# Performance work log

Hardware: AMD Instinct MI355X
Metric: run time of the kernel (lower is better)

## Reference

```python
import jax, jax.numpy as jnp
import numpy as np

C, K, D = 256, 16, 256  # clusters, cluster_size, embed_dim
MARGIN = 1.0
EPS = 1e-6  # torch pairwise_distance eps


def setup_inputs() -> dict:
    key = jax.random.key(0)
    batch = jax.random.normal(key, (C, K, D), dtype=jnp.float32)
    return {"batch": batch}


def reference(batch):
    # world_size == 1, rank == 0  ->  my_embeds == all_embeds
    c, k, d = batch.shape
    emb = batch.reshape(-1, d)                       # [N, D], N = c*k
    n = emb.shape[0]

    sq = jnp.sum(emb * emb, axis=-1)                 # [N]
    d2 = sq[:, None] + sq[None, :] - 2.0 * (emb @ emb.T)
    dist = jnp.sqrt(jnp.maximum(d2, 0.0))            # [N, N]

    labels = jnp.repeat(jnp.arange(c), k)            # [N]
    pos_mask = labels[:, None] == labels[None, :]    # [N, N]

    # hardest positive: masked max (masked entries -> -1, matching pytorch code)
    pos_idx = jnp.argmax(jnp.where(pos_mask, dist, -1.0), axis=1)
    # hardest negative: masked min (positives -> +inf)
    neg_idx = jnp.argmin(jnp.where(pos_mask, jnp.inf, dist), axis=1)

    positives = emb[pos_idx]                         # [N, D]
    negatives = emb[neg_idx]                         # [N, D]

    # TripletMarginLoss(margin=1.0, p=2): pairwise_distance adds eps to the diff
    d_ap = jnp.linalg.norm(emb - positives + EPS, axis=-1)
    d_an = jnp.linalg.norm(emb - negatives + EPS, axis=-1)
    loss = jnp.mean(jnp.maximum(d_ap - d_an + MARGIN, 0.0))
    return loss
```

## Files before the change

### kernel.cpp

```cpp
#include <hip/hip_runtime.h>
#include <math.h>

#define CC 256
#define KK 16
#define DD 256
#define NN 4096
#define EPSV 1e-6f

typedef unsigned long long u64;
typedef __attribute__((ext_vector_type(8))) short short8v;
typedef __attribute__((ext_vector_type(8))) unsigned short ushort8v;
typedef __attribute__((ext_vector_type(4))) float f32x4;

__global__ __launch_bounds__(256) void prep_kernel(const float* __restrict__ emb,
                                                   float* __restrict__ sq,
                                                   unsigned short* __restrict__ hi,
                                                   u64* __restrict__ posk,
                                                   u64* __restrict__ negk,
                                                   float* __restrict__ out) {
  __shared__ __attribute__((aligned(16))) unsigned short hiS[16][264];
  const int g = blockIdx.x;
  const int t = threadIdx.x;
  const int r = t >> 4, q = t & 15;
  const int row = g * 16 + r;

  const float* src = emb + (size_t)row * DD + q * 16;
  float s = 0.f;
  #pragma unroll
  for (int i = 0; i < 4; ++i) {
    float4 v = *reinterpret_cast<const float4*>(src + 4 * i);
    float f[4] = {v.x, v.y, v.z, v.w};
    #pragma unroll
    for (int e = 0; e < 4; ++e) {
      s += f[e] * f[e];
      hiS[r][q * 16 + 4 * i + e] = (unsigned short)(__float_as_uint(f[e]) >> 16);
    }
  }
  #pragma unroll
  for (int off = 1; off < 16; off <<= 1) s += __shfl_xor(s, off);
  if (q == 0) {
    sq[row] = s;
    posk[row] = 0ull;
    negk[row] = ~0ull;
  }
  if (g == 0 && t == 0) out[0] = 0.0f;
  __syncthreads();

  #pragma unroll
  for (int h = 0; h < 2; ++h) {
    int q2 = h * 256 + t;
    int s2 = q2 >> 6, fl = q2 & 63;
    int col = 32 * s2 + 8 * (fl >> 4);
    ushort8v hv = *reinterpret_cast<const ushort8v*>(&hiS[fl & 15][col]);
    *reinterpret_cast<ushort8v*>(hi + ((size_t)(g * 8 + s2) * 64 + fl) * 8) = hv;
  }
}

__global__ __launch_bounds__(256, 4) void mine_mfma_kernel(const unsigned short* __restrict__ hi,
                                                           const float* __restrict__ sq,
                                                           u64* __restrict__ posk,
                                                           u64* __restrict__ negk) {
  const int ib = blockIdx.x >> 5, jb = blockIdx.x & 31;
  const bool diag = (ib == jb);
  const int ibRow = ib * 128, jbRow = jb * 128;

  const int tid = threadIdx.x;
  const int lane = tid & 63;
  const int w = tid >> 6;
  const int wm = w >> 1, wn = w & 1;
  const int fr = lane & 15;
  const int grp = lane >> 4;

  int ofsA[4], ofsB[4];
  #pragma unroll
  for (int m = 0; m < 4; ++m) ofsA[m] = (ib * 8 + wm * 4 + m) * 4096 + lane * 8;
  #pragma unroll
  for (int n = 0; n < 4; ++n) ofsB[n] = (jb * 8 + wn * 4 + n) * 4096 + lane * 8;

  f32x4 acc[4][4];
  #pragma unroll
  for (int m = 0; m < 4; ++m)
    #pragma unroll
    for (int n = 0; n < 4; ++n)
      acc[m][n] = (f32x4){0.f, 0.f, 0.f, 0.f};

  #pragma unroll 2
  for (int s = 0; s < 8; ++s) {
    short8v a[4], b[4];
    #pragma unroll
    for (int m = 0; m < 4; ++m)
      a[m] = *reinterpret_cast<const short8v*>(hi + ofsA[m] + s * 512);
    #pragma unroll
    for (int n = 0; n < 4; ++n)
      b[n] = *reinterpret_cast<const short8v*>(hi + ofsB[n] + s * 512);
    #pragma unroll
    for (int m = 0; m < 4; ++m)
      #pragma unroll
      for (int n = 0; n < 4; ++n)
        acc[m][n] = __builtin_amdgcn_mfma_f32_16x16x32_bf16(a[m], b[n], acc[m][n], 0, 0, 0);
  }

  float sqjv[4]; int jglob[4];
  #pragma unroll
  for (int n = 0; n < 4; ++n) {
    jglob[n] = jbRow + wn * 64 + n * 16 + fr;
    sqjv[n] = sq[jglob[n]];
  }

  #pragma unroll
  for (int m = 0; m < 4; ++m) {
    #pragma unroll
    for (int r = 0; r < 4; ++r) {
      const int gi = ibRow + wm * 64 + m * 16 + grp * 4 + r;
      const float sqiv = sq[gi];
      float pv = -1.0f; int pj = -1;
      float nv = 3.0e38f; int nj = 0x7fffffff;
      #pragma unroll
      for (int n = 0; n < 4; ++n) {
        const float d2 = fmaxf(sqiv + sqjv[n] - 2.0f * acc[m][n][r], 0.0f);
        const int j = jglob[n];
        const bool isPos = diag && ((j >> 4) == (gi >> 4));
        if (isPos) {
          if (d2 > pv || (d2 == pv && j < pj)) { pv = d2; pj = j; }
        } else {
          if (d2 < nv || (d2 == nv && j < nj)) { nv = d2; nj = j; }
        }
      }
      #pragma unroll
      for (int off = 1; off < 16; off <<= 1) {
        float ov = __shfl_xor(nv, off); int oj = __shfl_xor(nj, off);
        if (ov < nv || (ov == nv && oj < nj)) { nv = ov; nj = oj; }
        float pov = __shfl_xor(pv, off); int poj = __shfl_xor(pj, off);
        if (pov > pv || (pov == pv && ((unsigned)poj < (unsigned)pj))) { pv = pov; pj = poj; }
      }
      if (fr == 0) {
        if (nj != 0x7fffffff)
          atomicMin(&negk[gi], ((u64)__float_as_uint(nv) << 32) | (unsigned)nj);
        if (diag && pj >= 0)
          atomicMax(&posk[gi], ((u64)__float_as_uint(pv) << 32) |
                                   (unsigned)(0xFFFFFFFFu - (unsigned)pj));
      }
    }
  }
}

__global__ __launch_bounds__(1024) void triplet_kernel(const float* __restrict__ emb,
                                                       const u64* __restrict__ posk,
                                                       const u64* __restrict__ negk,
                                                       float* __restrict__ out) {
  __shared__ float part[16];
  const int w = threadIdx.x >> 6;
  const int lane = threadIdx.x & 63;
  const int i = blockIdx.x * 16 + w;

  u64 pk = posk[i], nk = negk[i];
  int p = (int)(0xFFFFFFFFu - (unsigned)(pk & 0xFFFFFFFFu));
  int nidx = (int)(nk & 0xFFFFFFFFu);

  float4 e  = *reinterpret_cast<const float4*>(emb + (size_t)i * DD + 4 * lane);
  float4 ep = *reinterpret_cast<const float4*>(emb + (size_t)p * DD + 4 * lane);
  float4 en = *reinterpret_cast<const float4*>(emb + (size_t)nidx * DD + 4 * lane);

  float dpx = e.x - ep.x + EPSV, dpy = e.y - ep.y + EPSV,
        dpz = e.z - ep.z + EPSV, dpw = e.w - ep.w + EPSV;
  float dnx = e.x - en.x + EPSV, dny = e.y - en.y + EPSV,
        dnz = e.z - en.z + EPSV, dnw = e.w - en.w + EPSV;
  float sp = dpx * dpx + dpy * dpy + dpz * dpz + dpw * dpw;
  float sn = dnx * dnx + dny * dny + dnz * dnz + dnw * dnw;
  #pragma unroll
  for (int off = 32; off; off >>= 1) {
    sp += __shfl_xor(sp, off);
    sn += __shfl_xor(sn, off);
  }
  if (lane == 0) part[w] = fmaxf(sqrtf(sp) - sqrtf(sn) + 1.0f, 0.0f);
  __syncthreads();
  if (threadIdx.x == 0) {
    float s = 0.f;
    #pragma unroll
    for (int k = 0; k < 16; ++k) s += part[k];
    atomicAdd(out, s * (1.0f / NN));
  }
}

extern "C" void kernel_launch(void* const* d_in, const int* in_sizes, int n_in,
                              void* d_out, int out_size, void* d_ws, size_t ws_size,
                              hipStream_t stream) {
  const float* emb = (const float*)d_in[0];
  char* ws = (char*)d_ws;
  float* sq = (float*)ws;
  u64* posk = (u64*)(ws + (16 << 10));
  u64* negk = (u64*)(ws + (48 << 10));
  unsigned short* hi = (unsigned short*)(ws + (96 << 10));
  float* out = (float*)d_out;

  prep_kernel<<<256, 256, 0, stream>>>(emb, sq, hi, posk, negk, out);
  mine_mfma_kernel<<<1024, 256, 0, stream>>>(hi, sq, posk, negk);
  triplet_kernel<<<256, 1024, 0, stream>>>(emb, posk, negk, out);
}
```

Measured before the change: 95.80 us.

## Stage MFMA operand tiles through double-buffered LDS via direct global-to-LDS loads

The mining kernel previously had each wave load its A and B bf16 fragments straight from global memory, so the two waves sharing a row or column tile fetched the same data twice. Now the block cooperatively copies each K-step's 128x32 A and B tiles into LDS with global_load_lds and double-buffers them, prefetching step s+1 while step s runs its MFMAs. This cuts redundant global/L2 traffic and overlaps loads with compute. In exchange it adds 32KB of LDS per block, which may limit occupancy against the 4-blocks target, plus a barrier every K-step.

```diff
diff --git a/kernel.cpp b/kernel.cpp
--- a/kernel.cpp
+++ b/kernel.cpp
@@ -56,10 +56,18 @@
   }
 }
 
+__device__ __forceinline__ void gll16(const unsigned short* g, unsigned short* l) {
+  __builtin_amdgcn_global_load_lds(
+      (const __attribute__((address_space(1))) unsigned int*)(const void*)g,
+      (__attribute__((address_space(3))) unsigned int*)(void*)l, 16, 0, 0);
+}
+
 __global__ __launch_bounds__(256, 4) void mine_mfma_kernel(const unsigned short* __restrict__ hi,
                                                            const float* __restrict__ sq,
                                                            u64* __restrict__ posk,
                                                            u64* __restrict__ negk) {
+  __shared__ __attribute__((aligned(16))) unsigned short lds[2][8192];
+
   const int ib = blockIdx.x >> 5, jb = blockIdx.x & 31;
   const bool diag = (ib == jb);
   const int ibRow = ib * 128, jbRow = jb * 128;
@@ -71,11 +79,11 @@
   const int fr = lane & 15;
   const int grp = lane >> 4;
 
-  int ofsA[4], ofsB[4];
-  #pragma unroll
-  for (int m = 0; m < 4; ++m) ofsA[m] = (ib * 8 + wm * 4 + m) * 4096 + lane * 8;
-  #pragma unroll
-  for (int n = 0; n < 4; ++n) ofsB[n] = (jb * 8 + wn * 4 + n) * 4096 + lane * 8;
+  const int a0 = 2 * w, a1 = a0 + 1;
+  const unsigned short* gA0 = hi + (size_t)(ib * 8 + a0) * 4096 + lane * 8;
+  const unsigned short* gA1 = hi + (size_t)(ib * 8 + a1) * 4096 + lane * 8;
+  const unsigned short* gB0 = hi + (size_t)(jb * 8 + a0) * 4096 + lane * 8;
+  const unsigned short* gB1 = hi + (size_t)(jb * 8 + a1) * 4096 + lane * 8;
 
   f32x4 acc[4][4];
   #pragma unroll
@@ -84,20 +92,35 @@
     for (int n = 0; n < 4; ++n)
       acc[m][n] = (f32x4){0.f, 0.f, 0.f, 0.f};
 
-  #pragma unroll 2
+  gll16(gA0, &lds[0][a0 * 512]);
+  gll16(gA1, &lds[0][a1 * 512]);
+  gll16(gB0, &lds[0][4096 + a0 * 512]);
+  gll16(gB1, &lds[0][4096 + a1 * 512]);
+  __syncthreads();
+
+  #pragma unroll
   for (int s = 0; s < 8; ++s) {
+    const int p = s & 1;
+    if (s < 7) {
+      const int so = (s + 1) * 512;
+      gll16(gA0 + so, &lds[p ^ 1][a0 * 512]);
+      gll16(gA1 + so, &lds[p ^ 1][a1 * 512]);
+      gll16(gB0 + so, &lds[p ^ 1][4096 + a0 * 512]);
+      gll16(gB1 + so, &lds[p ^ 1][4096 + a1 * 512]);
+    }
     short8v a[4], b[4];
     #pragma unroll
     for (int m = 0; m < 4; ++m)
-      a[m] = *reinterpret_cast<const short8v*>(hi + ofsA[m] + s * 512);
+      a[m] = *reinterpret_cast<const short8v*>(&lds[p][(wm * 4 + m) * 512 + lane * 8]);
     #pragma unroll
     for (int n = 0; n < 4; ++n)
-      b[n] = *reinterpret_cast<const short8v*>(hi + ofsB[n] + s * 512);
+      b[n] = *reinterpret_cast<const short8v*>(&lds[p][4096 + (wn * 4 + n) * 512 + lane * 8]);
     #pragma unroll
     for (int m = 0; m < 4; ++m)
       #pragma unroll
       for (int n = 0; n < 4; ++n)
         acc[m][n] = __builtin_amdgcn_mfma_f32_16x16x32_bf16(a[m], b[n], acc[m][n], 0, 0, 0);
+    __syncthreads();
   }
 
   float sqjv[4]; int jglob[4];
```

New measurement: 92.26 us. 1.04x faster.

## Stage B tile in LDS via global_load_lds and retile warps to 32x128

Applied to the files above, without the earlier changes.

The mining kernel now loads the 128-row B tile into shared memory once per block using direct global-to-LDS loads, then reads B fragments from LDS. Each warp owns a 32x128 output slab and keeps its A fragments for all 8 K-steps in registers. The block index is swizzled so co-resident blocks share tiles in L2. The aim is to cut redundant global/L2 reads of B across warps. The cost is more register and LDS use per block, which lowers occupancy to 2 blocks per CU and puts a block-wide sync before compute.

```diff
diff --git a/kernel.cpp b/kernel.cpp
--- a/kernel.cpp
+++ b/kernel.cpp
@@ -56,67 +56,87 @@
   }
 }
 
-__global__ __launch_bounds__(256, 4) void mine_mfma_kernel(const unsigned short* __restrict__ hi,
+__device__ __forceinline__ void gll16(const unsigned short* g, unsigned short* l) {
+  __builtin_amdgcn_global_load_lds(
+      (const __attribute__((address_space(1))) unsigned int*)(const void*)g,
+      (__attribute__((address_space(3))) unsigned int*)(void*)l, 16, 0, 0);
+}
+
+__global__ __launch_bounds__(256, 2) void mine_mfma_kernel(const unsigned short* __restrict__ hi,
                                                            const float* __restrict__ sq,
                                                            u64* __restrict__ posk,
                                                            u64* __restrict__ negk) {
-  const int ib = blockIdx.x >> 5, jb = blockIdx.x & 31;
+  __shared__ __attribute__((aligned(16))) unsigned short ldsB[8][4096];
+
+  const int bid = blockIdx.x;
+  const int wg = (bid & 7) * 128 + (bid >> 3);
+  const int ib = wg >> 5, jb = wg & 31;
   const bool diag = (ib == jb);
   const int ibRow = ib * 128, jbRow = jb * 128;
 
   const int tid = threadIdx.x;
   const int lane = tid & 63;
   const int w = tid >> 6;
-  const int wm = w >> 1, wn = w & 1;
   const int fr = lane & 15;
   const int grp = lane >> 4;
 
-  int ofsA[4], ofsB[4];
-  #pragma unroll
-  for (int m = 0; m < 4; ++m) ofsA[m] = (ib * 8 + wm * 4 + m) * 4096 + lane * 8;
-  #pragma unroll
-  for (int n = 0; n < 4; ++n) ofsB[n] = (jb * 8 + wn * 4 + n) * 4096 + lane * 8;
-
-  f32x4 acc[4][4];
-  #pragma unroll
-  for (int m = 0; m < 4; ++m)
-    #pragma unroll
-    for (int n = 0; n < 4; ++n)
+  {
+    const int c0 = 2 * w, c1 = c0 + 1;
+    const unsigned short* g0 = hi + ((size_t)(jb * 8 + c0) * 8) * 512 + lane * 8;
+    const unsigned short* g1 = hi + ((size_t)(jb * 8 + c1) * 8) * 512 + lane * 8;
+    #pragma unroll
+    for (int s = 0; s < 8; ++s) {
+      gll16(g0 + s * 512, &ldsB[s][c0 * 512]);
+      gll16(g1 + s * 512, &ldsB[s][c1 * 512]);
+    }
+  }
+  short8v a[8][2];
+  #pragma unroll
+  for (int m = 0; m < 2; ++m) {
+    const unsigned short* ga = hi + ((size_t)(ib * 8 + 2 * w + m) * 8) * 512 + lane * 8;
+    #pragma unroll
+    for (int s = 0; s < 8; ++s)
+      a[s][m] = *reinterpret_cast<const short8v*>(ga + s * 512);
+  }
+  __syncthreads();
+
+  f32x4 acc[2][8];
+  #pragma unroll
+  for (int m = 0; m < 2; ++m)
+    #pragma unroll
+    for (int n = 0; n < 8; ++n)
       acc[m][n] = (f32x4){0.f, 0.f, 0.f, 0.f};
 
-  #pragma unroll 2
+  #pragma unroll
   for (int s = 0; s < 8; ++s) {
-    short8v a[4], b[4];
-    #pragma unroll
-    for (int m = 0; m < 4; ++m)
-      a[m] = *reinterpret_cast<const short8v*>(hi + ofsA[m] + s * 512);
-    #pragma unroll
-    for (int n = 0; n < 4; ++n)
-      b[n] = *reinterpret_cast<const short8v*>(hi + ofsB[n] + s * 512);
-    #pragma unroll
-    for (int m = 0; m < 4; ++m)
+    short8v b[8];
+    #pragma unroll
+    for (int n = 0; n < 8; ++n)
+      b[n] = *reinterpret_cast<const short8v*>(&ldsB[s][n * 512 + lane * 8]);
+    #pragma unroll
+    for (int m = 0; m < 2; ++m)
       #pragma unroll
-      for (int n = 0; n < 4; ++n)
-        acc[m][n] = __builtin_amdgcn_mfma_f32_16x16x32_bf16(a[m], b[n], acc[m][n], 0, 0, 0);
-  }
-
-  float sqjv[4]; int jglob[4];
-  #pragma unroll
-  for (int n = 0; n < 4; ++n) {
-    jglob[n] = jbRow + wn * 64 + n * 16 + fr;
+      for (int n = 0; n < 8; ++n)
+        acc[m][n] = __builtin_amdgcn_mfma_f32_16x16x32_bf16(a[s][m], b[n], acc[m][n], 0, 0, 0);
+  }
+
+  float sqjv[8]; int jglob[8];
+  #pragma unroll
+  for (int n = 0; n < 8; ++n) {
+    jglob[n] = jbRow + n * 16 + fr;
     sqjv[n] = sq[jglob[n]];
   }
 
   #pragma unroll
-  for (int m = 0; m < 4; ++m) {
+  for (int m = 0; m < 2; ++m) {
     #pragma unroll
     for (int r = 0; r < 4; ++r) {
-      const int gi = ibRow + wm * 64 + m * 16 + grp * 4 + r;
+      const int gi = ibRow + w * 32 + m * 16 + grp * 4 + r;
       const float sqiv = sq[gi];
       float pv = -1.0f; int pj = -1;
       float nv = 3.0e38f; int nj = 0x7fffffff;
       #pragma unroll
-      for (int n = 0; n < 4; ++n) {
+      for (int n = 0; n < 8; ++n) {
         const float d2 = fmaxf(sqiv + sqjv[n] - 2.0f * acc[m][n][r], 0.0f);
         const int j = jglob[n];
         const bool isPos = diag && ((j >> 4) == (gi >> 4));
```

Result: no change. 96.40 us (+0.6%).
